# Kernel tuning notes

Hardware: AMD Instinct MI355X
Metric: run time of the kernel (lower is better)

The kernel has to match this reference:

```python
import jax, jax.numpy as jnp
import numpy as np

N = 100000          # nodes
F_IN = 500          # num_features
HID = 256           # hidden
C = 40              # out_classes
E = 2302585         # ~ N*ln(N)*ec, doubled (both directions) in spar_samp
ALPHA0 = 0.1        # att[0][0] = alpha*(1-alpha)**0


def setup_inputs() -> dict:
    key = jax.random.key(0)
    ks = jax.random.split(key, 8)
    x = jax.random.normal(ks[0], (N, F_IN), dtype=jnp.float32)
    W1 = jax.random.normal(ks[1], (F_IN, HID), dtype=jnp.float32) * (1.0 / np.sqrt(F_IN))
    b1 = jnp.zeros((HID,), dtype=jnp.float32)
    W2 = jax.random.normal(ks[2], (HID, C), dtype=jnp.float32) * (1.0 / np.sqrt(HID))
    b2 = jnp.zeros((C,), dtype=jnp.float32)
    edge_row = jax.random.randint(ks[3], (E,), 0, N, dtype=jnp.int64) if jax.config.jax_enable_x64 else jax.random.randint(ks[3], (E,), 0, N, dtype=jnp.int32)
    edge_col = jax.random.randint(ks[4], (E,), 0, N, dtype=edge_row.dtype)
    # sampled importance weights: deg^{-1/2}*deg^{-1/2}*(M/num_edgess) -> small positive floats
    edge_val = jax.random.uniform(ks[5], (E,), dtype=jnp.float32, minval=0.001, maxval=0.05)
    return {"x": x, "W1": W1, "b1": b1, "W2": W2, "b2": b2,
            "edge_row": edge_row, "edge_col": edge_col, "edge_val": edge_val}


def reference(x, W1, b1, W2, b2, edge_row, edge_col, edge_val):
    # eval mode: dropout is identity
    h = jax.nn.relu(x @ W1 + b1)          # [N, HID]
    h = h @ W2 + b2                       # [N, C]
    # sparse propagation: out[r] += val * h[c]  (scatter-add SpMM)
    msg = edge_val[:, None] * h[edge_col]            # [E, C] gather
    agg = jax.ops.segment_sum(msg, edge_row, num_segments=N)  # [N, C]
    out = h * ALPHA0 + agg
    return jax.nn.log_softmax(out, axis=1)
```

## Files before the change

### kernel.cpp

```cpp
#include <hip/hip_runtime.h>
#include <hip/hip_bf16.h>


#define N_NODES 100000
#define F_IN    500
#define HID     256
#define C_OUT   40
#define ALPHA0  0.1f
#define H2STRIDE 64

#define RPB     64
#define NBUCK   ((N_NODES + RPB - 1) / RPB)
#define NCH     320
#define SCAN_M  (NBUCK * NCH)
#define SCAN_CHUNK 2048
#define NBS     ((SCAN_M + SCAN_CHUNK - 1) / SCAN_CHUNK)
#define BCAPL   1792

typedef short short8 __attribute__((ext_vector_type(8)));
typedef float f32x4  __attribute__((ext_vector_type(4)));

__device__ __forceinline__ short f2bf(float f) {
  union { float f; unsigned u; } x; x.f = f;
  unsigned r = x.u + 0x7fffu + ((x.u >> 16) & 1u);
  return (short)(r >> 16);
}
__device__ __forceinline__ float bf2f(short s) {
  union { unsigned u; float f; } x; x.u = ((unsigned)(unsigned short)s) << 16;
  return x.f;
}
__device__ __forceinline__ unsigned cvtpk(float lo, float hi) {
  unsigned r;
  asm("v_cvt_pk_bf16_f32 %0, %1, %2" : "=v"(r) : "v"(lo), "v"(hi));
  return r;
}
__device__ __forceinline__ void lbar() {
  asm volatile("s_waitcnt lgkmcnt(0)" ::: "memory");
  __builtin_amdgcn_s_barrier();
}
__device__ __forceinline__ void gll16(const float* g, const char* l) {
  __builtin_amdgcn_global_load_lds(
      (const __attribute__((address_space(1))) void*)g,
      (__attribute__((address_space(3))) void*)l, 16, 0, 0);
}

__global__ __launch_bounds__(256) void k_pack_weights(
    const float* __restrict__ W1, const float* __restrict__ W2,
    short* __restrict__ W1S, short* __restrict__ W2T)
{
  int i = blockIdx.x * 256 + threadIdx.x;
  if (i < 16*256*32) {
    int kc  = i >> 13;
    int idx = i & 8191;
    int n   = idx >> 5;
    int kk  = idx & 31;
    int k   = kc*32 + kk;
    float v = (k < F_IN) ? W1[k*HID + n] : 0.f;
    W1S[i] = f2bf(v);
  } else {
    int j = i - 16*256*32;
    if (j < 48*256) {
      int n = j >> 8;
      int k = j & 255;
      float v = (n < C_OUT) ? W2[k*C_OUT + n] : 0.f;
      W2T[j] = f2bf(v);
    }
  }
}

__global__ __launch_bounds__(512, 4) void k_fused_mlp(
    const float* __restrict__ x, const float* __restrict__ b1v,
    const float* __restrict__ b2v,
    const short* __restrict__ W1S, const short* __restrict__ W2T,
    short* __restrict__ h2b)
{
  __shared__ __align__(16) char smem[65536];
  short (*Hl)[256] = (short(*)[256])smem;

  const int tid  = threadIdx.x;
  const int w    = tid >> 6;
  const int lane = tid & 63;
  const int lr   = lane & 15;
  const int quad = lane >> 4;
  const int wr   = w >> 2;
  const int wc   = w & 3;
  const int row0 = blockIdx.x * 128;

  const int s_rl0 = (w*2)*8 + (lane>>3);
  const int s_rl1 = (w*2+1)*8 + (lane>>3);
  const int ksw   = ((lane&7) ^ ((lane>>3)&7)) * 4;
  const float* gp0 = x + (size_t)min(row0 + s_rl0, N_NODES-1) * F_IN;
  const float* gp1 = x + (size_t)min(row0 + s_rl1, N_NODES-1) * F_IN;
  const char* l0 = smem + (w*2)*1024;
  const char* l1 = smem + (w*2+1)*1024;

  f32x4 acc[4][4] = {};

  #pragma unroll
  for (int p = 0; p < 2; ++p) {
    int kb = p*32 + ksw;
    const float* a0 = (kb + 4 <= F_IN) ? gp0 + kb : x;
    const float* a1 = (kb + 4 <= F_IN) ? gp1 + kb : x;
    gll16(a0, l0 + p*16384);
    gll16(a1, l1 + p*16384);
  }

  const short* bbase = W1S + (wc*64 + lr)*32 + quad*8;
  const int m2 = lr & 7;

  #pragma unroll
  for (int kc = 0; kc < 16; ++kc) {
    short8 bf4[4];
    #pragma unroll
    for (int t = 0; t < 4; ++t)
      bf4[t] = *(const short8*)(bbase + kc*8192 + t*16*32);
    __builtin_amdgcn_sched_barrier(0);

    if (kc < 14) {
      int kb = (kc+2)*32 + ksw;
      const float* a0 = (kb + 4 <= F_IN) ? gp0 + kb : x;
      const float* a1 = (kb + 4 <= F_IN) ? gp1 + kb : x;
      gll16(a0, l0 + ((kc+2)&3)*16384);
      gll16(a1, l1 + ((kc+2)&3)*16384);
      __builtin_amdgcn_sched_barrier(0);
      asm volatile("s_waitcnt vmcnt(8)" ::: "memory");
    } else if (kc == 14) {
      asm volatile("s_waitcnt vmcnt(6)" ::: "memory");
    } else {
      asm volatile("s_waitcnt vmcnt(4)" ::: "memory");
    }
    __builtin_amdgcn_s_barrier();

    const char* Abase = smem + (kc & 3)*16384;
    short8 af[4];
    #pragma unroll
    for (int t = 0; t < 4; ++t) {
      int rl = wr*64 + t*16 + lr;
      f32x4 u0 = *(const f32x4*)(Abase + rl*128 + (((quad*2  ) ^ m2) << 4));
      f32x4 u1 = *(const f32x4*)(Abase + rl*128 + (((quad*2+1) ^ m2) << 4));
      union { unsigned u[4]; short8 s; } pk;
      pk.u[0] = cvtpk(u0[0], u0[1]);
      pk.u[1] = cvtpk(u0[2], u0[3]);
      pk.u[2] = cvtpk(u1[0], u1[1]);
      pk.u[3] = cvtpk(u1[2], u1[3]);
      af[t] = pk.s;
    }

    #pragma unroll
    for (int rt = 0; rt < 4; ++rt)
      #pragma unroll
      for (int ct = 0; ct < 4; ++ct)
        acc[rt][ct] = __builtin_amdgcn_mfma_f32_16x16x32_bf16(af[rt], bf4[ct], acc[rt][ct], 0, 0, 0);
  }
  lbar();

  #pragma unroll
  for (int ct = 0; ct < 4; ++ct) {
    int col = wc*64 + ct*16 + lr;
    int cg = col >> 3, ci = col & 7;
    float bias = b1v[col];
    #pragma unroll
    for (int rt = 0; rt < 4; ++rt) {
      #pragma unroll
      for (int r = 0; r < 4; ++r) {
        int row = wr*64 + rt*16 + quad*4 + r;
        float v = fmaxf(acc[rt][ct][r] + bias, 0.f);
        Hl[row][((cg ^ (row & 31)) << 3) | ci] = f2bf(v);
      }
    }
  }
  lbar();

  f32x4 acc2[3] = {};
  const int arow = w*16 + lr;
  #pragma unroll
  for (int kc2 = 0; kc2 < 8; ++kc2) {
    int gg = kc2*4 + quad;
    short8 a2 = *(const short8*)&Hl[arow][(gg ^ (arow & 31)) << 3];
    #pragma unroll
    for (int nt = 0; nt < 3; ++nt) {
      short8 b2 = *(const short8*)(W2T + (nt*16 + lr)*256 + kc2*32 + quad*8);
      acc2[nt] = __builtin_amdgcn_mfma_f32_16x16x32_bf16(a2, b2, acc2[nt], 0, 0, 0);
    }
  }

  #pragma unroll
  for (int nt = 0; nt < 3; ++nt) {
    int col = nt*16 + lr;
    float bias = (col < C_OUT) ? b2v[col] : 0.f;
    #pragma unroll
    for (int r = 0; r < 4; ++r) {
      int row = row0 + w*16 + quad*4 + r;
      if (row < N_NODES) {
        float v = (col < C_OUT) ? (acc2[nt][r] + bias) : 0.f;
        h2b[(long)row * H2STRIDE + col] = f2bf(v);
      }
    }
  }
  {
    int col = 48 + lr;
    #pragma unroll
    for (int r = 0; r < 4; ++r) {
      int row = row0 + w*16 + quad*4 + r;
      if (row < N_NODES) h2b[(long)row * H2STRIDE + col] = 0;
    }
  }
}

__global__ __launch_bounds__(256) void k_hist2(
    const int* __restrict__ erow, int* __restrict__ offs, int E, int CH)
{
  __shared__ int h[NBUCK];
  int tid = threadIdx.x, c = blockIdx.x;
  for (int b = tid; b < NBUCK; b += 256) h[b] = 0;
  __syncthreads();
  int e0 = c * CH, e1 = min(E, e0 + CH);
  for (int e = e0 + tid; e < e1; e += 256)
    atomicAdd(&h[erow[e] >> 6], 1);
  __syncthreads();
  for (int b = tid; b < NBUCK; b += 256) offs[b * NCH + c] = h[b];
}

__global__ __launch_bounds__(256) void k_scan1(
    int* __restrict__ offs, int* __restrict__ bsums)
{
  __shared__ int sh[256];
  int tid = threadIdx.x;
  int base = blockIdx.x * SCAN_CHUNK + tid * 8;
  int d[8];
  #pragma unroll
  for (int k = 0; k < 8; ++k)
    d[k] = (base + k < SCAN_M) ? offs[base + k] : 0;
  int s = 0;
  #pragma unroll
  for (int k = 0; k < 8; ++k) s += d[k];
  sh[tid] = s;
  __syncthreads();
  for (int o = 1; o < 256; o <<= 1) {
    int v = (tid >= o) ? sh[tid - o] : 0;
    __syncthreads();
    if (tid >= o) sh[tid] += v;
    __syncthreads();
  }
  int run = sh[tid] - s;
  #pragma unroll
  for (int k = 0; k < 8; ++k) {
    if (base + k < SCAN_M) offs[base + k] = run;
    run += d[k];
  }
  if (tid == 255) bsums[blockIdx.x] = sh[255];
}

__global__ __launch_bounds__(256) void k_split(
    const int* __restrict__ erow, const int* __restrict__ ecol,
    const float* __restrict__ eval, const int* __restrict__ offs,
    const int* __restrict__ bsums, int2* __restrict__ sorted,
    int* __restrict__ bstart, int E, int CH)
{
  __shared__ int P[256];
  __shared__ int cur[NBUCK];
  int tid = threadIdx.x, c = blockIdx.x;

  int v = (tid < NBS) ? bsums[tid] : 0;
  P[tid] = v;
  __syncthreads();
  for (int o = 1; o < 256; o <<= 1) {
    int u = (tid >= o) ? P[tid - o] : 0;
    __syncthreads();
    if (tid >= o) P[tid] += u;
    __syncthreads();
  }
  int incl = P[tid];
  __syncthreads();
  P[tid] = incl - v;
  __syncthreads();

  for (int b = tid; b < NBUCK; b += 256) {
    int m = b * NCH + c;
    int val = offs[m] + P[m >> 11];
    cur[b] = val;
    if (c == 0) bstart[b] = val;
  }
  if (c == 0 && tid == 0) bstart[NBUCK] = E;
  __syncthreads();

  int e0 = c * CH, e1 = min(E, e0 + CH);
  for (int e = e0 + tid; e < e1; e += 256) {
    int r = erow[e];
    int b = r >> 6;
    int pos = atomicAdd(&cur[b], 1);
    int2 cv;
    cv.x = ecol[e] | ((r & 63) << 17);
    cv.y = __float_as_int(eval[e]);
    sorted[pos] = cv;
  }
}

__global__ __launch_bounds__(256) void k_csr_spmm(
    const int* __restrict__ bstart, const int2* __restrict__ sorted,
    const short* __restrict__ h2b, float* __restrict__ out)
{
  __shared__ int2 eS[BCAPL];
  __shared__ int h[RPB];
  __shared__ int roff[RPB];
  __shared__ int cur[RPB];
  int tid = threadIdx.x, b = blockIdx.x;
  int lane = tid & 63, w = tid >> 6;
  int start = bstart[b], end = bstart[b + 1];
  int cnt = end - start;

  int2 cv[7];
  int nloc = 0;
  for (int i = tid, k = 0; i < cnt; i += 256, ++k) { cv[k] = sorted[start + i]; nloc = k + 1; }

  if (tid < RPB) h[tid] = 0;
  __syncthreads();
  for (int k = 0; k < nloc; ++k)
    atomicAdd(&h[((unsigned)cv[k].x) >> 17], 1);
  __syncthreads();
  if (tid < RPB) roff[tid] = h[tid];
  __syncthreads();
  for (int o = 1; o < RPB; o <<= 1) {
    int u = (tid >= o && tid < RPB) ? roff[tid - o] : 0;
    __syncthreads();
    if (tid >= o && tid < RPB) roff[tid] += u;
    __syncthreads();
  }
  if (tid < RPB) cur[tid] = roff[tid] - h[tid];
  __syncthreads();
  for (int k = 0; k < nloc; ++k) {
    unsigned rl = ((unsigned)cv[k].x) >> 17;
    int p = atomicAdd(&cur[rl], 1);
    if (p < BCAPL) eS[p] = cv[k];
  }
  __syncthreads();

  for (int rr = 0; rr < 16; ++rr) {
    int r = w * 16 + rr;
    int row = b * RPB + r;
    if (row >= N_NODES) continue;
    float acc = ALPHA0 * bf2f(h2b[(size_t)row * H2STRIDE + lane]);
    int e  = roff[r] - h[r];
    int ee = roff[r];
    for (; e + 3 < ee; e += 4) {
      int2 c0 = eS[e], c1 = eS[e+1], c2 = eS[e+2], c3 = eS[e+3];
      float g0 = bf2f(h2b[(size_t)(c0.x & 0x1FFFF) * H2STRIDE + lane]);
      float g1 = bf2f(h2b[(size_t)(c1.x & 0x1FFFF) * H2STRIDE + lane]);
      float g2 = bf2f(h2b[(size_t)(c2.x & 0x1FFFF) * H2STRIDE + lane]);
      float g3 = bf2f(h2b[(size_t)(c3.x & 0x1FFFF) * H2STRIDE + lane]);
      acc += __int_as_float(c0.y) * g0;
      acc += __int_as_float(c1.y) * g1;
      acc += __int_as_float(c2.y) * g2;
      acc += __int_as_float(c3.y) * g3;
    }
    for (; e < ee; ++e) {
      int2 c0 = eS[e];
      acc += __int_as_float(c0.y) * bf2f(h2b[(size_t)(c0.x & 0x1FFFF) * H2STRIDE + lane]);
    }
    float m = (lane < C_OUT) ? acc : -INFINITY;
    #pragma unroll
    for (int o = 32; o > 0; o >>= 1) m = fmaxf(m, __shfl_xor(m, o));
    float ev = (lane < C_OUT) ? __expf(acc - m) : 0.f;
    float s = ev;
    #pragma unroll
    for (int o = 32; o > 0; o >>= 1) s += __shfl_xor(s, o);
    if (lane < C_OUT) out[(long)row * C_OUT + lane] = acc - m - __logf(s);
  }
}

extern "C" void kernel_launch(void* const* d_in, const int* in_sizes, int n_in,
                              void* d_out, int out_size, void* d_ws, size_t ws_size,
                              hipStream_t stream) {
  const float* x    = (const float*)d_in[0];
  const float* W1   = (const float*)d_in[1];
  const float* b1   = (const float*)d_in[2];
  const float* W2   = (const float*)d_in[3];
  const float* b2   = (const float*)d_in[4];
  const int*   erow = (const int*)d_in[5];
  const int*   ecol = (const int*)d_in[6];
  const float* eval = (const float*)d_in[7];
  const int E  = in_sizes[5];
  const int CH = (E + NCH - 1) / NCH;

  char* p = (char*)d_ws;
  short* h2b    = (short*)p;  p += (size_t)N_NODES * H2STRIDE * 2;
  short* W1S    = (short*)p;  p += (size_t)16*256*32 * 2;
  short* W2T    = (short*)p;  p += (size_t)48*256 * 2;
  int*   offs   = (int*)p;    p += (size_t)SCAN_M * 4;
  int*   bsums  = (int*)p;    p += 256 * 4;
  int*   bstart = (int*)p;    p += (size_t)(NBUCK + 4) * 4;
  int2*  sorted = (int2*)p;
  float* out = (float*)d_out;

  k_pack_weights<<<(16*256*32 + 48*256 + 255)/256, 256, 0, stream>>>(W1, W2, W1S, W2T);
  k_fused_mlp<<<(N_NODES + 127)/128, 512, 0, stream>>>(x, b1, b2, W1S, W2T, h2b);
  k_hist2<<<NCH, 256, 0, stream>>>(erow, offs, E, CH);
  k_scan1<<<NBS, 256, 0, stream>>>(offs, bsums);
  k_split<<<NCH, 256, 0, stream>>>(erow, ecol, eval, offs, bsums, sorted, bstart, E, CH);
  k_csr_spmm<<<NBUCK, 256, 0, stream>>>(bstart, sorted, h2b, out);
}
```

Baseline: 528.5 us.

## Raise edge-chunk count, vectorize histogram/split loads, add separate scan pass, unroll SpMM gather

The number of edge chunks for the bucket sort rises from 320 to 1024, giving more blocks in the histogram and split kernels, and the chunk size is rounded to a multiple of 4. Both kernels now read row, col and value arrays as int4/float4 vectors. Because the block-sum count now exceeds 256, a new single-block kernel scans the block sums instead of each split block rescanning them. The SpMM inner loop gets an 8-wide unrolled gather so more loads are in flight. The cost is a larger offsets array, more scan work and one extra launch.

```diff
diff --git a/kernel.cpp b/kernel.cpp
--- a/kernel.cpp
+++ b/kernel.cpp
@@ -11,7 +11,7 @@
 
 #define RPB     64
 #define NBUCK   ((N_NODES + RPB - 1) / RPB)
-#define NCH     320
+#define NCH     1024
 #define SCAN_M  (NBUCK * NCH)
 #define SCAN_CHUNK 2048
 #define NBS     ((SCAN_M + SCAN_CHUNK - 1) / SCAN_CHUNK)
@@ -215,8 +215,19 @@
   for (int b = tid; b < NBUCK; b += 256) h[b] = 0;
   __syncthreads();
   int e0 = c * CH, e1 = min(E, e0 + CH);
-  for (int e = e0 + tid; e < e1; e += 256)
-    atomicAdd(&h[erow[e] >> 6], 1);
+  if (e0 < e1) {
+    int g0 = e0 >> 2, g1 = e1 >> 2;
+    const int4* rp = (const int4*)erow;
+    for (int g = g0 + tid; g < g1; g += 256) {
+      int4 r4 = rp[g];
+      atomicAdd(&h[r4.x >> 6], 1);
+      atomicAdd(&h[r4.y >> 6], 1);
+      atomicAdd(&h[r4.z >> 6], 1);
+      atomicAdd(&h[r4.w >> 6], 1);
+    }
+    for (int e = (g1 << 2) + tid; e < e1; e += 256)
+      atomicAdd(&h[erow[e] >> 6], 1);
+  }
   __syncthreads();
   for (int b = tid; b < NBUCK; b += 256) offs[b * NCH + c] = h[b];
 }
@@ -249,6 +260,34 @@
     run += d[k];
   }
   if (tid == 255) bsums[blockIdx.x] = sh[255];
+}
+
+__global__ __launch_bounds__(256) void k_scan2(int* __restrict__ bsums) {
+  __shared__ int sh[256];
+  int tid = threadIdx.x;
+  int d[4];
+  int s = 0;
+  #pragma unroll
+  for (int k = 0; k < 4; ++k) {
+    int i = tid * 4 + k;
+    d[k] = (i < NBS) ? bsums[i] : 0;
+    s += d[k];
+  }
+  sh[tid] = s;
+  __syncthreads();
+  for (int o = 1; o < 256; o <<= 1) {
+    int u = (tid >= o) ? sh[tid - o] : 0;
+    __syncthreads();
+    if (tid >= o) sh[tid] += u;
+    __syncthreads();
+  }
+  int run = sh[tid] - s;
+  #pragma unroll
+  for (int k = 0; k < 4; ++k) {
+    int i = tid * 4 + k;
+    if (i < NBS) bsums[i] = run;
+    run += d[k];
+  }
 }
 
 __global__ __launch_bounds__(256) void k_split(
@@ -257,27 +296,12 @@
     const int* __restrict__ bsums, int2* __restrict__ sorted,
     int* __restrict__ bstart, int E, int CH)
 {
-  __shared__ int P[256];
   __shared__ int cur[NBUCK];
   int tid = threadIdx.x, c = blockIdx.x;
 
-  int v = (tid < NBS) ? bsums[tid] : 0;
-  P[tid] = v;
-  __syncthreads();
-  for (int o = 1; o < 256; o <<= 1) {
-    int u = (tid >= o) ? P[tid - o] : 0;
-    __syncthreads();
-    if (tid >= o) P[tid] += u;
-    __syncthreads();
-  }
-  int incl = P[tid];
-  __syncthreads();
-  P[tid] = incl - v;
-  __syncthreads();
-
   for (int b = tid; b < NBUCK; b += 256) {
     int m = b * NCH + c;
-    int val = offs[m] + P[m >> 11];
+    int val = offs[m] + bsums[m >> 11];
     cur[b] = val;
     if (c == 0) bstart[b] = val;
   }
@@ -285,10 +309,28 @@
   __syncthreads();
 
   int e0 = c * CH, e1 = min(E, e0 + CH);
-  for (int e = e0 + tid; e < e1; e += 256) {
+  if (e0 >= e1) return;
+  int g0 = e0 >> 2, g1 = e1 >> 2;
+  const int4*   rp = (const int4*)erow;
+  const int4*   cp = (const int4*)ecol;
+  const float4* vp = (const float4*)eval;
+  for (int g = g0 + tid; g < g1; g += 256) {
+    int4 r4 = rp[g];
+    int4 c4 = cp[g];
+    float4 v4 = vp[g];
+    int p0 = atomicAdd(&cur[r4.x >> 6], 1);
+    int p1 = atomicAdd(&cur[r4.y >> 6], 1);
+    int p2 = atomicAdd(&cur[r4.z >> 6], 1);
+    int p3 = atomicAdd(&cur[r4.w >> 6], 1);
+    int2 cv;
+    cv.x = c4.x | ((r4.x & 63) << 17); cv.y = __float_as_int(v4.x); sorted[p0] = cv;
+    cv.x = c4.y | ((r4.y & 63) << 17); cv.y = __float_as_int(v4.y); sorted[p1] = cv;
+    cv.x = c4.z | ((r4.z & 63) << 17); cv.y = __float_as_int(v4.z); sorted[p2] = cv;
+    cv.x = c4.w | ((r4.w & 63) << 17); cv.y = __float_as_int(v4.w); sorted[p3] = cv;
+  }
+  for (int e = (g1 << 2) + tid; e < e1; e += 256) {
     int r = erow[e];
-    int b = r >> 6;
-    int pos = atomicAdd(&cur[b], 1);
+    int pos = atomicAdd(&cur[r >> 6], 1);
     int2 cv;
     cv.x = ecol[e] | ((r & 63) << 17);
     cv.y = __float_as_int(eval[e]);
@@ -342,6 +384,17 @@
     float acc = ALPHA0 * bf2f(h2b[(size_t)row * H2STRIDE + lane]);
     int e  = roff[r] - h[r];
     int ee = roff[r];
+    for (; e + 7 < ee; e += 8) {
+      int2 cc[8];
+      float gg[8];
+      #pragma unroll
+      for (int j = 0; j < 8; ++j) cc[j] = eS[e + j];
+      #pragma unroll
+      for (int j = 0; j < 8; ++j)
+        gg[j] = bf2f(h2b[(size_t)(cc[j].x & 0x1FFFF) * H2STRIDE + lane]);
+      #pragma unroll
+      for (int j = 0; j < 8; ++j) acc += __int_as_float(cc[j].y) * gg[j];
+    }
     for (; e + 3 < ee; e += 4) {
       int2 c0 = eS[e], c1 = eS[e+1], c2 = eS[e+2], c3 = eS[e+3];
       float g0 = bf2f(h2b[(size_t)(c0.x & 0x1FFFF) * H2STRIDE + lane]);
@@ -380,14 +433,15 @@
   const int*   ecol = (const int*)d_in[6];
   const float* eval = (const float*)d_in[7];
   const int E  = in_sizes[5];
-  const int CH = (E + NCH - 1) / NCH;
+  int CH = (E + NCH - 1) / NCH;
+  CH = (CH + 3) & ~3;
 
   char* p = (char*)d_ws;
   short* h2b    = (short*)p;  p += (size_t)N_NODES * H2STRIDE * 2;
   short* W1S    = (short*)p;  p += (size_t)16*256*32 * 2;
   short* W2T    = (short*)p;  p += (size_t)48*256 * 2;
   int*   offs   = (int*)p;    p += (size_t)SCAN_M * 4;
-  int*   bsums  = (int*)p;    p += 256 * 4;
+  int*   bsums  = (int*)p;    p += 1024 * 4;
   int*   bstart = (int*)p;    p += (size_t)(NBUCK + 4) * 4;
   int2*  sorted = (int2*)p;
   float* out = (float*)d_out;
@@ -396,6 +450,7 @@
   k_fused_mlp<<<(N_NODES + 127)/128, 512, 0, stream>>>(x, b1, b2, W1S, W2T, h2b);
   k_hist2<<<NCH, 256, 0, stream>>>(erow, offs, E, CH);
   k_scan1<<<NBS, 256, 0, stream>>>(offs, bsums);
+  k_scan2<<<1, 256, 0, stream>>>(bsums);
   k_split<<<NCH, 256, 0, stream>>>(erow, ecol, eval, offs, bsums, sorted, bstart, E, CH);
   k_csr_spmm<<<NBUCK, 256, 0, stream>>>(bstart, sorted, h2b, out);
 }
```

Result: faster. 505.6 us (-4.3%).
